# Optimization experiments

Hardware: AMD Instinct MI355X
Metric: run time of the kernel (lower is better)

## Reference

```python
import jax, jax.numpy as jnp
import numpy as np

EPS = 1e-5  # BatchNorm1d default eps


def _gcn_layer(x, src, dst, ew, W, b, N):
    # PyG GCNConv: h = x @ W, add self-loops (weight 1), symmetric norm, aggregate at dst, + bias
    h = x @ W
    loop = jnp.arange(N)
    src_a = jnp.concatenate([src, loop])
    dst_a = jnp.concatenate([dst, loop])
    ew_a = jnp.concatenate([ew, jnp.ones((N,), x.dtype)])
    deg = jax.ops.segment_sum(ew_a, dst_a, num_segments=N)  # [N]
    dinv = jax.lax.rsqrt(deg)  # deg >= 1 thanks to self-loops
    norm = dinv[src_a] * ew_a * dinv[dst_a]  # [E+N]
    out = jax.ops.segment_sum(h[src_a] * norm[:, None], dst_a, num_segments=N)
    return out + b


def _bn_relu(h, gamma, beta):
    # training-mode BatchNorm1d over the node dimension (biased variance)
    mean = h.mean(axis=0)
    var = jnp.mean((h - mean) ** 2, axis=0)
    return jax.nn.relu((h - mean) * jax.lax.rsqrt(var + EPS) * gamma + beta)


def setup_inputs() -> dict:
    key = jax.random.key(0)
    ks = jax.random.split(key, 8)
    N, E, D, H = 100000, 1600000, 64, 64
    x = jax.random.normal(ks[0], (N, D), dtype=jnp.float32)
    edge_index = jax.random.randint(ks[1], (2, E), 0, N, dtype=jnp.int64)
    edge_weight = jax.random.uniform(ks[2], (E,), dtype=jnp.float32)
    s = 1.0 / np.sqrt(D)
    W1 = jax.random.uniform(ks[3], (D, H), jnp.float32, -s, s)
    b1 = jnp.zeros((H,), jnp.float32)
    gamma1 = jnp.ones((H,), jnp.float32)
    beta1 = jnp.zeros((H,), jnp.float32)
    s2 = 1.0 / np.sqrt(H)
    W2 = jax.random.uniform(ks[4], (H, H), jnp.float32, -s2, s2)
    b2 = jnp.zeros((H,), jnp.float32)
    gamma2 = jnp.ones((H,), jnp.float32)
    beta2 = jnp.zeros((H,), jnp.float32)
    return {"x": x, "edge_index": edge_index, "edge_weight": edge_weight,
            "W1": W1, "b1": b1, "gamma1": gamma1, "beta1": beta1,
            "W2": W2, "b2": b2, "gamma2": gamma2, "beta2": beta2}


def reference(x, edge_index, edge_weight, W1, b1, gamma1, beta1, W2, b2, gamma2, beta2):
    N = x.shape[0]
    src, dst = edge_index[0], edge_index[1]  # messages flow src -> dst
    h = _gcn_layer(x, src, dst, edge_weight, W1, b1, N)
    h = _bn_relu(h, gamma1, beta1)
    h = _gcn_layer(h, src, dst, edge_weight, W2, b2, N)
    h = _bn_relu(h, gamma2, beta2)
    return h
```

## Files before the change

### kernel.cpp

```cpp
#include <hip/hip_runtime.h>
#include <hip/hip_fp16.h>


#define NPB   200
#define NBMAX 512
#define CAP   5120
#define CHUNK 8192

typedef unsigned long long u64;

__global__ __launch_bounds__(512) void k_init(int* gcur, float* stats) {
  int t = threadIdx.x;
  if (t < NBMAX) gcur[t] = 0;
  if (t < 256) stats[t] = 0.f;
}

__global__ __launch_bounds__(256) void k_bucket(const int* __restrict__ ei,
                                                const float* __restrict__ ew,
                                                int* gcur, u64* __restrict__ bkt,
                                                int E, int NB) {
  __shared__ int lcnt[NBMAX];
  __shared__ int lbase[NBMAX];
  int t = threadIdx.x;
  for (int b = t; b < NBMAX; b += 256) lcnt[b] = 0;
  __syncthreads();
  int lo = blockIdx.x * CHUNK;
  int hi = min(lo + CHUNK, E);
  for (int i = lo + t; i < hi; i += 256)
    atomicAdd(&lcnt[ei[E + i] / NPB], 1);
  __syncthreads();
  for (int b = t; b < NB; b += 256) {
    int c = lcnt[b];
    lbase[b] = c ? atomicAdd(&gcur[b], c) : 0;
    lcnt[b] = 0;
  }
  __syncthreads();
  for (int i = lo + t; i < hi; i += 256) {
    int src = ei[i], dst = ei[E + i];
    float w = ew[i];
    int b = dst / NPB;
    int pos = lbase[b] + atomicAdd(&lcnt[b], 1);
    if (pos < CAP) {
      unsigned wq = (unsigned)(w * 1073741824.0f);
      if (wq > 0x3FFFFFFFu) wq = 0x3FFFFFFFu;
      bkt[(size_t)b * CAP + pos] =
          ((u64)(unsigned)dst << 47) | ((u64)(unsigned)src << 30) | (u64)wq;
    }
  }
}

__global__ __launch_bounds__(256) void k_sort(const u64* __restrict__ bkt,
                                              const int* __restrict__ gcur,
                                              float2* __restrict__ csr,
                                              int2* __restrict__ row,
                                              float* __restrict__ dinv, int N) {
  __shared__ u64 sorted[CAP];
  __shared__ int hist[256];
  __shared__ int offs[256];
  __shared__ int cur[NPB];
  __shared__ int cpArr[NPB];
  __shared__ float dv[NPB];
  int b = blockIdx.x, t = threadIdx.x;
  for (int i = t; i < CAP; i += 256) sorted[i] = 0ULL;
  hist[t] = 0;
  if (t < NPB) cur[t] = 0;
  __syncthreads();
  int cnt = min(gcur[b], CAP);
  size_t base = (size_t)b * CAP;
  for (int i = t; i < cnt; i += 256) {
    int dl = (int)(bkt[base + i] >> 47) - b * NPB;
    atomicAdd(&hist[dl], 1);
  }
  __syncthreads();
  int c = (t < NPB) ? ((hist[t] + 7) & ~7) : 0;
  offs[t] = c;
  __syncthreads();
  for (int o = 1; o < 256; o <<= 1) {
    int x = (t >= o) ? offs[t - o] : 0;
    __syncthreads();
    offs[t] += x;
    __syncthreads();
  }
  int total = offs[255];
  int myoff = offs[t] - c;
  __syncthreads();
  offs[t] = myoff;
  if (t < NPB) cpArr[t] = c;
  __syncthreads();
  for (int i = t; i < cnt; i += 256) {
    u64 u = bkt[base + i];
    int dl = (int)(u >> 47) - b * NPB;
    int pos = offs[dl] + atomicAdd(&cur[dl], 1);
    if (pos < CAP) sorted[pos] = u;
  }
  __syncthreads();
  for (int q = t; q < NPB * 4; q += 256) {
    int n = q >> 2, s = q & 3;
    int o = offs[n], cp = cpArr[n];
    float sum = 0.f;
    for (int j = o + s; j < o + cp; j += 4)
      sum += (float)(unsigned)(sorted[j] & 0x3FFFFFFFu);
    sum += __shfl_xor(sum, 1);
    sum += __shfl_xor(sum, 2);
    if (s == 0) {
      float d = rsqrtf(sum * (1.0f / 1073741824.0f) + 1.0f);
      dv[n] = d;
      int gn = b * NPB + n;
      if (gn < N) dinv[gn] = d;
    }
  }
  __syncthreads();
  int totalC = min(total, CAP);
  for (int j = t; j < totalC; j += 256) {
    u64 u = sorted[j];
    unsigned wq = (unsigned)(u & 0x3FFFFFFFu);
    int dl = (int)(u >> 47) - b * NPB;
    int dlc = (wq == 0) ? 0 : dl;
    float w = (float)wq * (1.0f / 1073741824.0f) * dv[dlc];
    int s = (int)((u >> 30) & 0x1FFFFu);
    csr[base + j] = make_float2(__int_as_float(s), w);
  }
  for (int n = t; n < NPB; n += 256) {
    int gn = b * NPB + n;
    if (gn < N) {
      int o = offs[n];
      int cp = min(cpArr[n], max(0, CAP - o)) & ~7;
      row[gn] = make_int2((int)(base + o), cp);
    }
  }
}

__device__ inline unsigned pk2(float a, float b) {
  __half2 h = __floats2half2_rn(a, b);
  return *reinterpret_cast<unsigned*>(&h);
}

template <int FUSE>
__global__ __launch_bounds__(256) void k_gemm(const float* __restrict__ X,
                                              const float* __restrict__ W,
                                              __half* __restrict__ Y, int N,
                                              const float* __restrict__ scale,
                                              const float* __restrict__ shift) {
  __shared__ float Wl[64 * 64];
  __shared__ float sc[64], sh[64];
  int tid = threadIdx.x;
  {
    float4* Wl4 = (float4*)Wl;
    const float4* W4 = (const float4*)W;
#pragma unroll
    for (int i = 0; i < 4; ++i) Wl4[tid + i * 256] = W4[tid + i * 256];
  }
  if (FUSE && tid < 64) { sc[tid] = scale[tid]; sh[tid] = shift[tid]; }
  __syncthreads();
  int row = blockIdx.x * 64 + (tid >> 2);
  if (row >= N) return;
  int c0 = (tid & 3) * 16;
  float4 a0 = make_float4(0.f, 0.f, 0.f, 0.f), a1 = a0, a2 = a0, a3 = a0;
  const float4* Xr = (const float4*)(X + (size_t)row * 64);
#pragma unroll
  for (int kk = 0; kk < 16; ++kk) {
    float4 xv = Xr[kk];
    if (FUSE) {
      int k4 = kk * 4;
      xv.x = fmaxf(fmaf(xv.x, sc[k4 + 0], sh[k4 + 0]), 0.f);
      xv.y = fmaxf(fmaf(xv.y, sc[k4 + 1], sh[k4 + 1]), 0.f);
      xv.z = fmaxf(fmaf(xv.z, sc[k4 + 2], sh[k4 + 2]), 0.f);
      xv.w = fmaxf(fmaf(xv.w, sc[k4 + 3], sh[k4 + 3]), 0.f);
    }
    const float* wbase = &Wl[(kk * 4) * 64 + c0];
#pragma unroll
    for (int d = 0; d < 4; ++d) {
      float xk = (d == 0) ? xv.x : (d == 1) ? xv.y : (d == 2) ? xv.z : xv.w;
      const float4* Wr = (const float4*)(wbase + d * 64);
      float4 w0 = Wr[0], w1 = Wr[1], w2 = Wr[2], w3 = Wr[3];
      a0.x = fmaf(xk, w0.x, a0.x); a0.y = fmaf(xk, w0.y, a0.y);
      a0.z = fmaf(xk, w0.z, a0.z); a0.w = fmaf(xk, w0.w, a0.w);
      a1.x = fmaf(xk, w1.x, a1.x); a1.y = fmaf(xk, w1.y, a1.y);
      a1.z = fmaf(xk, w1.z, a1.z); a1.w = fmaf(xk, w1.w, a1.w);
      a2.x = fmaf(xk, w2.x, a2.x); a2.y = fmaf(xk, w2.y, a2.y);
      a2.z = fmaf(xk, w2.z, a2.z); a2.w = fmaf(xk, w2.w, a2.w);
      a3.x = fmaf(xk, w3.x, a3.x); a3.y = fmaf(xk, w3.y, a3.y);
      a3.z = fmaf(xk, w3.z, a3.z); a3.w = fmaf(xk, w3.w, a3.w);
    }
  }
  uint4 p0, p1;
  p0.x = pk2(a0.x, a0.y); p0.y = pk2(a0.z, a0.w);
  p0.z = pk2(a1.x, a1.y); p0.w = pk2(a1.z, a1.w);
  p1.x = pk2(a2.x, a2.y); p1.y = pk2(a2.z, a2.w);
  p1.z = pk2(a3.x, a3.y); p1.w = pk2(a3.z, a3.w);
  uint4* Y4 = (uint4*)(Y + (size_t)row * 64 + c0);
  Y4[0] = p0; Y4[1] = p1;
}

__global__ __launch_bounds__(256) void k_agg(const __half* __restrict__ H,
                                             const int2* __restrict__ row,
                                             const float2* __restrict__ csr,
                                             const float* __restrict__ dinv,
                                             const float* __restrict__ bias,
                                             float* __restrict__ out,
                                             float* __restrict__ sums,
                                             float* __restrict__ sumsq, int N) {
  int lane = threadIdx.x & 63;
  int wib = threadIdx.x >> 6;
  int wid = blockIdx.x * 4 + wib;
  int nw = gridDim.x * 4;
  float b = bias[lane];
  float ssum = 0.f, ssq = 0.f;
  for (int n = wid; n < N; n += nw) {
    int2 r = row[n];
    size_t base = (size_t)r.x;
    int cntp = r.y;
    float di = dinv[n];
    float hn = __half2float(H[(size_t)n * 64 + lane]);
    float acc0 = 0.f, acc1 = 0.f, acc2 = 0.f, acc3 = 0.f;
    const float4* c4 = (const float4*)(csr + base);
    for (int j = 0; j < cntp; j += 8) {
      float4 q0 = c4[(j >> 1) + 0], q1 = c4[(j >> 1) + 1];
      float4 q2 = c4[(j >> 1) + 2], q3 = c4[(j >> 1) + 3];
      int s0 = __float_as_int(q0.x), s1 = __float_as_int(q0.z);
      int s2 = __float_as_int(q1.x), s3 = __float_as_int(q1.z);
      int s4 = __float_as_int(q2.x), s5 = __float_as_int(q2.z);
      int s6 = __float_as_int(q3.x), s7 = __float_as_int(q3.z);
      float w0 = q0.y * dinv[s0], w1 = q0.w * dinv[s1];
      float w2 = q1.y * dinv[s2], w3 = q1.w * dinv[s3];
      float w4 = q2.y * dinv[s4], w5 = q2.w * dinv[s5];
      float w6 = q3.y * dinv[s6], w7 = q3.w * dinv[s7];
      float h0 = __half2float(H[(size_t)s0 * 64 + lane]);
      float h1 = __half2float(H[(size_t)s1 * 64 + lane]);
      float h2 = __half2float(H[(size_t)s2 * 64 + lane]);
      float h3 = __half2float(H[(size_t)s3 * 64 + lane]);
      float h4 = __half2float(H[(size_t)s4 * 64 + lane]);
      float h5 = __half2float(H[(size_t)s5 * 64 + lane]);
      float h6 = __half2float(H[(size_t)s6 * 64 + lane]);
      float h7 = __half2float(H[(size_t)s7 * 64 + lane]);
      acc0 = fmaf(w0, h0, acc0); acc1 = fmaf(w1, h1, acc1);
      acc2 = fmaf(w2, h2, acc2); acc3 = fmaf(w3, h3, acc3);
      acc0 = fmaf(w4, h4, acc0); acc1 = fmaf(w5, h5, acc1);
      acc2 = fmaf(w6, h6, acc2); acc3 = fmaf(w7, h7, acc3);
    }
    float v = (acc0 + acc1) + (acc2 + acc3) + di * di * hn + b;
    out[(size_t)n * 64 + lane] = v;
    ssum += v;
    ssq = fmaf(v, v, ssq);
  }
  __shared__ float ls[4][64];
  __shared__ float ls2[4][64];
  ls[wib][lane] = ssum; ls2[wib][lane] = ssq;
  __syncthreads();
  if (wib == 0) {
    float a = ls[0][lane] + ls[1][lane] + ls[2][lane] + ls[3][lane];
    float c = ls2[0][lane] + ls2[1][lane] + ls2[2][lane] + ls2[3][lane];
    atomicAdd(&sums[lane], a);
    atomicAdd(&sumsq[lane], c);
  }
}

__global__ __launch_bounds__(64) void k_finalize(const float* __restrict__ sums,
                                                 const float* __restrict__ sumsq,
                                                 const float* __restrict__ gamma,
                                                 const float* __restrict__ beta,
                                                 float* __restrict__ scale,
                                                 float* __restrict__ shift, float invN) {
  int t = threadIdx.x;
  if (t < 64) {
    float mean = sums[t] * invN;
    float var = sumsq[t] * invN - mean * mean;
    float sc = gamma[t] * rsqrtf(var + 1e-5f);
    scale[t] = sc;
    shift[t] = fmaf(-mean, sc, beta[t]);
  }
}

__global__ __launch_bounds__(256) void k_bnrelu(float* __restrict__ Y,
                                                const float* __restrict__ scale,
                                                const float* __restrict__ shift, int n4) {
  int i = blockIdx.x * 256 + threadIdx.x;
  if (i >= n4) return;
  float4 v = ((float4*)Y)[i];
  int f = (i & 15) * 4;
  v.x = fmaxf(fmaf(v.x, scale[f + 0], shift[f + 0]), 0.f);
  v.y = fmaxf(fmaf(v.y, scale[f + 1], shift[f + 1]), 0.f);
  v.z = fmaxf(fmaf(v.z, scale[f + 2], shift[f + 2]), 0.f);
  v.w = fmaxf(fmaf(v.w, scale[f + 3], shift[f + 3]), 0.f);
  ((float4*)Y)[i] = v;
}

extern "C" void kernel_launch(void* const* d_in, const int* in_sizes, int n_in,
                              void* d_out, int out_size, void* d_ws, size_t ws_size,
                              hipStream_t stream) {
  const float* x   = (const float*)d_in[0];
  const int*   ei  = (const int*)d_in[1];
  const float* ew  = (const float*)d_in[2];
  const float* W1  = (const float*)d_in[3];
  const float* b1  = (const float*)d_in[4];
  const float* g1  = (const float*)d_in[5];
  const float* be1 = (const float*)d_in[6];
  const float* W2  = (const float*)d_in[7];
  const float* b2  = (const float*)d_in[8];
  const float* g2  = (const float*)d_in[9];
  const float* be2 = (const float*)d_in[10];
  int N = in_sizes[0] / 64;
  int E = in_sizes[1] / 2;
  float* out = (float*)d_out;

  int NB = (N + NPB - 1) / NPB;

  char* ws = (char*)d_ws;
  size_t off = 0;
  auto alloc = [&](size_t bytes) {
    char* p = ws + off;
    off = (off + bytes + 255) & ~(size_t)255;
    return p;
  };

  int*    gcur  = (int*)alloc(NBMAX * 4);
  float*  dinv  = (float*)alloc((size_t)N * 4);
  __half* h1    = (__half*)alloc((size_t)N * 64 * 2);
  float*  stats = (float*)alloc(256 * 4);
  float*  scsh  = (float*)alloc(256 * 4);
  int2*   row   = (int2*)alloc((size_t)N * 8);
  u64*    bkt   = (u64*)alloc((size_t)NB * CAP * 8);
  float2* csr   = (float2*)alloc((size_t)NB * CAP * 8);

  float *sums1 = stats, *sumsq1 = stats + 64, *sums2 = stats + 128, *sumsq2 = stats + 192;
  float *scale1 = scsh, *shift1 = scsh + 64, *scale2 = scsh + 128, *shift2 = scsh + 192;

  k_init<<<1, 512, 0, stream>>>(gcur, stats);
  k_bucket<<<(E + CHUNK - 1) / CHUNK, 256, 0, stream>>>(ei, ew, gcur, bkt, E, NB);
  k_sort<<<NB, 256, 0, stream>>>(bkt, gcur, csr, row, dinv, N);

  k_gemm<0><<<(N + 63) / 64, 256, 0, stream>>>(x, W1, h1, N, nullptr, nullptr);
  k_agg<<<2048, 256, 0, stream>>>(h1, row, csr, dinv, b1, out, sums1, sumsq1, N);
  k_finalize<<<1, 64, 0, stream>>>(sums1, sumsq1, g1, be1, scale1, shift1, 1.0f / N);

  k_gemm<1><<<(N + 63) / 64, 256, 0, stream>>>(out, W2, h1, N, scale1, shift1);
  k_agg<<<2048, 256, 0, stream>>>(h1, row, csr, dinv, b2, out, sums2, sumsq2, N);
  k_finalize<<<1, 64, 0, stream>>>(sums2, sumsq2, g2, be2, scale2, shift2, 1.0f / N);
  k_bnrelu<<<(N * 16 + 255) / 256, 256, 0, stream>>>(out, scale2, shift2, N * 16);
}
```

Baseline: 307.1 us.

## Pack CSR entries into 32-bit src+quantized weight with pre-folded source dinv

Each CSR entry is now a single 32-bit word holding a 17-bit source index and a 15-bit fixed-point normalized weight, replacing the 8-byte float2. A new k_fold pass multiplies in dinv[src] once, so the aggregation loops no longer do a random gather of dinv per edge. The CSR stream is read with nontemporal loads and the output is written with nontemporal stores. This halves edge-list traffic and removes per-edge dinv lookups, at the cost of an extra kernel, 15-bit weight precision, and an index limit of 2^17 nodes.

```diff
diff --git a/kernel.cpp b/kernel.cpp
--- a/kernel.cpp
+++ b/kernel.cpp
@@ -8,6 +8,8 @@
 #define CHUNK 8192
 
 typedef unsigned long long u64;
+typedef unsigned int u32;
+typedef u32 u32x4 __attribute__((ext_vector_type(4)));
 
 __global__ __launch_bounds__(512) void k_init(int* gcur, float* stats) {
   int t = threadIdx.x;
@@ -51,7 +53,7 @@
 
 __global__ __launch_bounds__(256) void k_sort(const u64* __restrict__ bkt,
                                               const int* __restrict__ gcur,
-                                              float2* __restrict__ csr,
+                                              u32* __restrict__ csr,
                                               int2* __restrict__ row,
                                               float* __restrict__ dinv, int N) {
   __shared__ u64 sorted[CAP];
@@ -117,8 +119,10 @@
     int dl = (int)(u >> 47) - b * NPB;
     int dlc = (wq == 0) ? 0 : dl;
     float w = (float)wq * (1.0f / 1073741824.0f) * dv[dlc];
-    int s = (int)((u >> 30) & 0x1FFFFu);
-    csr[base + j] = make_float2(__int_as_float(s), w);
+    unsigned q15 = (unsigned)(w * 32768.0f + 0.5f);
+    if (q15 > 32767u) q15 = 32767u;
+    unsigned s = (unsigned)((u >> 30) & 0x1FFFFu);
+    csr[base + j] = (s << 15) | q15;
   }
   for (int n = t; n < NPB; n += 256) {
     int gn = b * NPB + n;
@@ -128,6 +132,23 @@
       row[gn] = make_int2((int)(base + o), cp);
     }
   }
+}
+
+__global__ __launch_bounds__(256) void k_fold(u32* __restrict__ csr,
+                                              const float* __restrict__ dinv,
+                                              int total4, int N) {
+  int i = blockIdx.x * 256 + threadIdx.x;
+  if (i >= total4) return;
+  uint4 q = ((uint4*)csr)[i];
+#pragma unroll
+  for (int k = 0; k < 4; ++k) {
+    u32 u = (&q.x)[k];
+    int s = (int)(u >> 15);
+    float d = dinv[min(s, N - 1)];
+    unsigned nq = (unsigned)((float)(u & 0x7FFFu) * d + 0.5f);
+    (&q.x)[k] = (u & 0xFFFF8000u) | nq;
+  }
+  ((uint4*)csr)[i] = q;
 }
 
 __device__ inline unsigned pk2(float a, float b) {
@@ -194,12 +215,13 @@
 
 __global__ __launch_bounds__(256) void k_agg(const __half* __restrict__ H,
                                              const int2* __restrict__ row,
-                                             const float2* __restrict__ csr,
+                                             const u32* __restrict__ csr,
                                              const float* __restrict__ dinv,
                                              const float* __restrict__ bias,
                                              float* __restrict__ out,
                                              float* __restrict__ sums,
                                              float* __restrict__ sumsq, int N) {
+  const float QS = 1.0f / 32768.0f;
   int lane = threadIdx.x & 63;
   int wib = threadIdx.x >> 6;
   int wid = blockIdx.x * 4 + wib;
@@ -208,23 +230,22 @@
   float ssum = 0.f, ssq = 0.f;
   for (int n = wid; n < N; n += nw) {
     int2 r = row[n];
-    size_t base = (size_t)r.x;
+    const u32x4* c4 = (const u32x4*)(csr + r.x);
     int cntp = r.y;
     float di = dinv[n];
     float hn = __half2float(H[(size_t)n * 64 + lane]);
     float acc0 = 0.f, acc1 = 0.f, acc2 = 0.f, acc3 = 0.f;
-    const float4* c4 = (const float4*)(csr + base);
     for (int j = 0; j < cntp; j += 8) {
-      float4 q0 = c4[(j >> 1) + 0], q1 = c4[(j >> 1) + 1];
-      float4 q2 = c4[(j >> 1) + 2], q3 = c4[(j >> 1) + 3];
-      int s0 = __float_as_int(q0.x), s1 = __float_as_int(q0.z);
-      int s2 = __float_as_int(q1.x), s3 = __float_as_int(q1.z);
-      int s4 = __float_as_int(q2.x), s5 = __float_as_int(q2.z);
-      int s6 = __float_as_int(q3.x), s7 = __float_as_int(q3.z);
-      float w0 = q0.y * dinv[s0], w1 = q0.w * dinv[s1];
-      float w2 = q1.y * dinv[s2], w3 = q1.w * dinv[s3];
-      float w4 = q2.y * dinv[s4], w5 = q2.w * dinv[s5];
-      float w6 = q3.y * dinv[s6], w7 = q3.w * dinv[s7];
+      u32x4 qa = __builtin_nontemporal_load(&c4[(j >> 2) + 0]);
+      u32x4 qb = __builtin_nontemporal_load(&c4[(j >> 2) + 1]);
+      int s0 = (int)(qa.x >> 15), s1 = (int)(qa.y >> 15);
+      int s2 = (int)(qa.z >> 15), s3 = (int)(qa.w >> 15);
+      int s4 = (int)(qb.x >> 15), s5 = (int)(qb.y >> 15);
+      int s6 = (int)(qb.z >> 15), s7 = (int)(qb.w >> 15);
+      float w0 = (float)(qa.x & 0x7FFFu) * QS, w1 = (float)(qa.y & 0x7FFFu) * QS;
+      float w2 = (float)(qa.z & 0x7FFFu) * QS, w3 = (float)(qa.w & 0x7FFFu) * QS;
+      float w4 = (float)(qb.x & 0x7FFFu) * QS, w5 = (float)(qb.y & 0x7FFFu) * QS;
+      float w6 = (float)(qb.z & 0x7FFFu) * QS, w7 = (float)(qb.w & 0x7FFFu) * QS;
       float h0 = __half2float(H[(size_t)s0 * 64 + lane]);
       float h1 = __half2float(H[(size_t)s1 * 64 + lane]);
       float h2 = __half2float(H[(size_t)s2 * 64 + lane]);
@@ -239,7 +260,7 @@
       acc2 = fmaf(w6, h6, acc2); acc3 = fmaf(w7, h7, acc3);
     }
     float v = (acc0 + acc1) + (acc2 + acc3) + di * di * hn + b;
-    out[(size_t)n * 64 + lane] = v;
+    __builtin_nontemporal_store(v, &out[(size_t)n * 64 + lane]);
     ssum += v;
     ssq = fmaf(v, v, ssq);
   }
@@ -320,14 +341,17 @@
   float*  scsh  = (float*)alloc(256 * 4);
   int2*   row   = (int2*)alloc((size_t)N * 8);
   u64*    bkt   = (u64*)alloc((size_t)NB * CAP * 8);
-  float2* csr   = (float2*)alloc((size_t)NB * CAP * 8);
+  u32*    csr   = (u32*)alloc((size_t)NB * CAP * 4);
 
   float *sums1 = stats, *sumsq1 = stats + 64, *sums2 = stats + 128, *sumsq2 = stats + 192;
   float *scale1 = scsh, *shift1 = scsh + 64, *scale2 = scsh + 128, *shift2 = scsh + 192;
+
+  int total4 = NB * CAP / 4;
 
   k_init<<<1, 512, 0, stream>>>(gcur, stats);
   k_bucket<<<(E + CHUNK - 1) / CHUNK, 256, 0, stream>>>(ei, ew, gcur, bkt, E, NB);
   k_sort<<<NB, 256, 0, stream>>>(bkt, gcur, csr, row, dinv, N);
+  k_fold<<<(total4 + 255) / 256, 256, 0, stream>>>(csr, dinv, total4, N);
 
   k_gemm<0><<<(N + 63) / 64, 256, 0, stream>>>(x, W1, h1, N, nullptr, nullptr);
   k_agg<<<2048, 256, 0, stream>>>(h1, row, csr, dinv, b1, out, sums1, sumsq1, N);
```

Result: no change. 302.2 us (-1.6%).
